# Kernel optimization log

Hardware: AMD Instinct MI355X
Metric: run time of the kernel (lower is better)

The kernel has to match this reference:

```python
import jax, jax.numpy as jnp
import numpy as np

B, S, D = 4, 2048, 1024
NH, NKV = 16, 4
HD = D // NH  # 64


def _rope(x, freqs):
    # x: [B, H, S, HD], freqs: [B, S, HD//2]
    cos = jnp.concatenate([jnp.cos(freqs), jnp.cos(freqs)], axis=-1)[:, None]  # [B,1,S,HD]
    sin = jnp.concatenate([jnp.sin(freqs), jnp.sin(freqs)], axis=-1)[:, None]
    x1, x2 = x[..., : HD // 2], x[..., HD // 2:]
    rot = jnp.concatenate([-x2, x1], axis=-1)
    return x * cos + rot * sin


def setup_inputs() -> dict:
    key = jax.random.key(0)
    ks = jax.random.split(key, 9)
    return {
        "hidden_states": jax.random.normal(ks[0], (B, S, D), jnp.float32),
        "rotary_pos_emb": jax.random.normal(ks[1], (B, S, HD // 2), jnp.float32),
        "Wq": jax.random.normal(ks[2], (D, NH * HD), jnp.float32) * 0.02,
        "bq": jax.random.normal(ks[3], (NH * HD,), jnp.float32) * 0.02,
        "Wk": jax.random.normal(ks[4], (D, NKV * HD), jnp.float32) * 0.02,
        "bk": jax.random.normal(ks[5], (NKV * HD,), jnp.float32) * 0.02,
        "Wv": jax.random.normal(ks[6], (D, NKV * HD), jnp.float32) * 0.02,
        "bv": jax.random.normal(ks[7], (NKV * HD,), jnp.float32) * 0.02,
        "Wo": jax.random.normal(ks[8], (NH * HD, D), jnp.float32) * 0.02,
    }


def reference(hidden_states, rotary_pos_emb, Wq, bq, Wk, bk, Wv, bv, Wo):
    b, s, _ = hidden_states.shape
    # projections -> [B, H, S, HD]
    q = (hidden_states @ Wq + bq).reshape(b, s, NH, HD).transpose(0, 2, 1, 3)
    k = (hidden_states @ Wk + bk).reshape(b, s, NKV, HD).transpose(0, 2, 1, 3)
    v = (hidden_states @ Wv + bv).reshape(b, s, NKV, HD).transpose(0, 2, 1, 3)
    q = _rope(q, rotary_pos_emb)
    k = _rope(k, rotary_pos_emb)
    groups = NH // NKV
    k = jnp.repeat(k, groups, axis=1)  # [B, NH, S, HD]
    v = jnp.repeat(v, groups, axis=1)
    scaling = HD ** -0.5
    scores = jnp.einsum("bhqd,bhkd->bhqk", q, k) * scaling
    probs = jax.nn.softmax(scores.astype(jnp.float32), axis=-1).astype(q.dtype)
    out = jnp.einsum("bhqk,bhkd->bhqd", probs, v)
    out = out.transpose(0, 2, 1, 3).reshape(b, s, NH * HD)
    return out @ Wo
```

## Files before the change

### kernel.cpp

```cpp
#include <hip/hip_runtime.h>
#include <hip/hip_bf16.h>

#define BB 4
#define SS 2048
#define DD 1024
#define NH 16
#define NKV 4
#define HD 64
#define MROWS (BB*SS)
#define NQKV (NH*HD + 2*NKV*HD)
#define KOFF (NH*HD)

typedef short v8s __attribute__((ext_vector_type(8)));
typedef short v4s __attribute__((ext_vector_type(4)));
typedef float v4f __attribute__((ext_vector_type(4)));
typedef unsigned short u16;
typedef unsigned int u32;

__device__ __forceinline__ float bf2f(u16 u){
  union { float f; u32 i; } x; x.i = ((u32)u) << 16; return x.f;
}
__device__ __forceinline__ u16 f2bf(float f){
  union { __hip_bfloat16 h; u16 u; } x; x.h = __float2bfloat16(f); return x.u;
}
__device__ __forceinline__ u32 cvtpk(float lo, float hi){
  u32 r;
  asm("v_cvt_pk_bf16_f32 %0, %1, %2" : "=v"(r) : "v"(lo), "v"(hi));
  return r;
}
__device__ __forceinline__ float fmax3(float a, float b, float c){
  return fmaxf(fmaxf(a, b), c);
}
__device__ __forceinline__ void gl_lds16(const u16* g, u16* l){
  __builtin_amdgcn_global_load_lds(
      (const __attribute__((address_space(1))) u32*)g,
      (__attribute__((address_space(3))) u32*)l, 16, 0, 0);
}


__global__ void build_bqkv(const float* __restrict__ Wq, const float* __restrict__ Wk,
                           const float* __restrict__ Wv, const float* __restrict__ bq,
                           const float* __restrict__ bk, const float* __restrict__ bv,
                           u16* __restrict__ Bt, float* __restrict__ bias){
  int idx = blockIdx.x*256 + threadIdx.x;
  int n = idx >> 10, k = idx & 1023;
  float v;
  if (n < 1024)      v = Wq[k*1024 + n];
  else if (n < 1280) v = Wk[k*256 + (n-1024)];
  else               v = Wv[k*256 + (n-1280)];
  Bt[idx] = f2bf(v);
  if (k == 0) bias[n] = (n < 1024) ? bq[n] : (n < 1280 ? bk[n-1024] : bv[n-1280]);
}

__global__ void build_wo(const float* __restrict__ Wo, u16* __restrict__ Bt){
  int idx = blockIdx.x*256 + threadIdx.x;
  int n = idx >> 10, k = idx & 1023;
  Bt[idx] = f2bf(Wo[k*1024 + n]);
}

__global__ void build_trig(const float* __restrict__ fr, float2* __restrict__ trig){
  int i = blockIdx.x*256 + threadIdx.x;
  float f = fr[i];
  float sn, cs; __sincosf(f, &sn, &cs);
  trig[i] = make_float2(cs, sn);
}

__global__ void rope_k(u16* __restrict__ QKV, const float* __restrict__ fr){
  int idx = blockIdx.x*256 + threadIdx.x;
  int d  = idx & 31;
  int hh = (idx >> 5) & 3;
  long row = idx >> 7;
  int col = KOFF + hh*HD + d;
  u16* p = QKV + row*NQKV;
  float x1 = bf2f(p[col]);
  float x2 = bf2f(p[col+32]);
  float f = fr[row*32 + d];
  float sn, cs; __sincosf(f, &sn, &cs);
  p[col]    = f2bf(x1*cs - x2*sn);
  p[col+32] = f2bf(x2*cs + x1*sn);
}


template<bool BIAS, typename IT, typename OT>
__global__ __launch_bounds__(256) void gemm_bt(
    const IT* __restrict__ A, const u16* __restrict__ Bt,
    const float* __restrict__ bias, OT* __restrict__ C,
    int K, int ldc)
{
  __shared__ u16 As[128*32];
  __shared__ u16 Bs[128*32];
  const int tid = threadIdx.x;
  const int wid = tid >> 6, lane = tid & 63;
  const int g = lane >> 4, c = lane & 15;
  const long brow = (long)blockIdx.y * 128;
  const long bcol = (long)blockIdx.x * 128;
  const int wr = (wid >> 1) * 64, wc = (wid & 1) * 64;
  const int srow = tid >> 2;
  const int scol = (tid & 3) * 8;
  const IT*  ga = &A [(brow + srow)*K + scol];
  const u16* gb = &Bt[(bcol + srow)*K + scol];
  u16* la  = &As[(wid*64)*8];
  u16* lb  = &Bs[(wid*64)*8];
  u16* lwa = &As[srow*32 + scol];
  v4f acc[4][4] = {};
  for (int kt = 0; kt < K; kt += 32) {
    __syncthreads();
    gl_lds16(gb + kt,        lb);
    gl_lds16(gb + 64*K + kt, lb + 256*8);
    if constexpr (sizeof(IT) == 4) {
      float4 a0 = *reinterpret_cast<const float4*>(ga + kt);
      float4 a1 = *reinterpret_cast<const float4*>(ga + kt + 4);
      float4 a2 = *reinterpret_cast<const float4*>(ga + (long)64*K + kt);
      float4 a3 = *reinterpret_cast<const float4*>(ga + (long)64*K + kt + 4);
      union { v8s v; u32 w[4]; } p0, p1;
      p0.w[0] = cvtpk(a0.x, a0.y); p0.w[1] = cvtpk(a0.z, a0.w);
      p0.w[2] = cvtpk(a1.x, a1.y); p0.w[3] = cvtpk(a1.z, a1.w);
      p1.w[0] = cvtpk(a2.x, a2.y); p1.w[1] = cvtpk(a2.z, a2.w);
      p1.w[2] = cvtpk(a3.x, a3.y); p1.w[3] = cvtpk(a3.z, a3.w);
      *reinterpret_cast<v8s*>(lwa)          = p0.v;
      *reinterpret_cast<v8s*>(lwa + 64*32)  = p1.v;
    } else {
      gl_lds16((const u16*)ga + kt,        la);
      gl_lds16((const u16*)ga + 64*K + kt, la + 256*8);
    }
    __syncthreads();
    v8s af[4], bf[4];
    #pragma unroll
    for (int m=0;m<4;m++) af[m] = *reinterpret_cast<const v8s*>(&As[(wr + m*16 + c)*32 + g*8]);
    #pragma unroll
    for (int n=0;n<4;n++) bf[n] = *reinterpret_cast<const v8s*>(&Bs[(wc + n*16 + c)*32 + g*8]);
    __builtin_amdgcn_s_setprio(1);
    #pragma unroll
    for (int m=0;m<4;m++)
      #pragma unroll
      for (int n=0;n<4;n++)
        acc[m][n] = __builtin_amdgcn_mfma_f32_16x16x32_bf16(af[m], bf[n], acc[m][n], 0,0,0);
    __builtin_amdgcn_s_setprio(0);
  }
  #pragma unroll
  for (int m=0;m<4;m++)
    #pragma unroll
    for (int n=0;n<4;n++) {
      int col = (int)bcol + wc + n*16 + c;
      float badd = BIAS ? bias[col] : 0.0f;
      #pragma unroll
      for (int r2=0;r2<4;r2++){
        long row = brow + wr + m*16 + g*4 + r2;
        float v = acc[m][n][r2] + badd;
        if constexpr (sizeof(OT)==2) C[row*ldc + col] = (OT)f2bf(v);
        else                         C[row*ldc + col] = (OT)v;
      }
    }
}


__global__ __launch_bounds__(512) void attn_k(const u16* __restrict__ QKV,
                                              const float2* __restrict__ trig,
                                              u16* __restrict__ Out){
  __shared__ u16 Ks[2][64][64];
  __shared__ u16 Vs[2][64][72];
  const int tid = threadIdx.x;
  const int wid = tid >> 6, lane = tid & 63;
  const int g = lane >> 4, c = lane & 15;
  const int qt = blockIdx.x & 7;
  const int bh = blockIdx.x >> 3;
  const int b = bh >> 4, h = bh & 15;
  const int kvh = h >> 2;
  const u16* Qb = QKV + (long)b*SS*NQKV + h*HD;
  const u16* Kb = QKV + (long)b*SS*NQKV + KOFF + kvh*HD;
  const u16* Vb = Kb + NKV*HD;

  const float SCL = 0.125f * 1.44269504088896f;
  v8s qf[2][2];
  #pragma unroll
  for (int qn=0;qn<2;qn++){
    int lrow = qt*256 + wid*32 + qn*16 + c;
    v8s q0 = *reinterpret_cast<const v8s*>(&Qb[(long)lrow*NQKV + g*8]);
    v8s q1 = *reinterpret_cast<const v8s*>(&Qb[(long)lrow*NQKV + 32 + g*8]);
    const float2* tp = trig + ((long)b*SS + lrow)*32 + g*8;
    union { v8s v; u32 w[4]; } a0, a1;
    #pragma unroll
    for (int wi=0;wi<4;wi++){
      float2 ta = tp[2*wi], tb = tp[2*wi+1];
      float x1a = bf2f((u16)q0[2*wi]),   x2a = bf2f((u16)q1[2*wi]);
      float x1b = bf2f((u16)q0[2*wi+1]), x2b = bf2f((u16)q1[2*wi+1]);
      float r0a = (x1a*ta.x - x2a*ta.y) * SCL;
      float r1a = (x2a*ta.x + x1a*ta.y) * SCL;
      float r0b = (x1b*tb.x - x2b*tb.y) * SCL;
      float r1b = (x2b*tb.x + x1b*tb.y) * SCL;
      a0.w[wi] = cvtpk(r0a, r0b);
      a1.w[wi] = cvtpk(r1a, r1b);
    }
    qf[qn][0] = a0.v; qf[qn][1] = a1.v;
  }

  v8s onesf;
  {
    short ov = (c==0) ? (short)0x3F80 : (short)0;
    #pragma unroll
    for (int j=0;j<8;j++) onesf[j] = ov;
  }

  v4f o[2][5] = {};
  float mr[2] = {0.f, 0.f};

  const int kgrow = wid*8 + (lane >> 3);
  const int kgchk = (lane & 7) ^ (lane >> 3);
  const u16* kp = Kb + (long)kgrow*NQKV + kgchk*8;
  u16* kdst0 = &Ks[0][wid*8][0];
  u16* kdst1 = &Ks[1][wid*8][0];

  const int key0 = 2*(tid >> 4);
  const int dg4  = (tid & 15) * 4;
  const int slot0 = 32*(key0>>5) + 8*((key0>>2)&3) + 4*((key0>>4)&1) + (key0&3);
  int vofs[4];
  #pragma unroll
  for (int j=0;j<4;j++){
    int d = dg4 + j;
    int idx = (((slot0>>3) ^ (d>>3)) << 3) | (slot0 & 7);
    vofs[j] = d*72 + idx;
  }
  u16* VsF = &Vs[0][0][0];

  const u16* vp0 = Vb + (long)key0*NQKV + dg4;
  const u16* vp1 = vp0 + NQKV;

  union { v4s v; u32 w[2]; } vr0, vr1;

  {
    gl_lds16(kp, kdst0);
    vr0.v = *reinterpret_cast<const v4s*>(vp0);
    vr1.v = *reinterpret_cast<const v4s*>(vp1);
    #pragma unroll
    for (int j=0;j<4;j++){
      u32 pkd = __builtin_amdgcn_perm(vr1.w[j>>1], vr0.w[j>>1],
                                      (j&1) ? 0x07060302u : 0x05040100u);
      *reinterpret_cast<u32*>(&VsF[vofs[j]]) = pkd;
    }
  }
  __syncthreads();

  int p = 0;
  for (int t = 0; t < SS/64; ++t){
    if (t+1 < SS/64) {
      long off = (long)(t+1)*64*NQKV;
      gl_lds16(kp + off, p ? kdst0 : kdst1);
      vr0.v = *reinterpret_cast<const v4s*>(vp0 + off);
      vr1.v = *reinterpret_cast<const v4s*>(vp1 + off);
    }

    v4f st[4][2];
    #pragma unroll
    for (int qn=0;qn<2;qn++){
      v4f mi = {-mr[qn], -mr[qn], -mr[qn], -mr[qn]};
      #pragma unroll
      for (int km=0;km<4;km++) st[km][qn] = mi;
    }
    #pragma unroll
    for (int ks=0;ks<2;ks++){
      v8s kf[4];
      #pragma unroll
      for (int km=0;km<4;km++)
        kf[km] = *reinterpret_cast<const v8s*>(
            &Ks[p][km*16 + c][(((ks*4 + g) ^ (c & 7)))*8]);
      __builtin_amdgcn_s_setprio(1);
      #pragma unroll
      for (int km=0;km<4;km++)
        #pragma unroll
        for (int qn=0;qn<2;qn++)
          st[km][qn] = __builtin_amdgcn_mfma_f32_16x16x32_bf16(kf[km], qf[qn][ks], st[km][qn], 0,0,0);
      __builtin_amdgcn_s_setprio(0);
    }

    float al[2];
    bool upd[2];
    #pragma unroll
    for (int qn=0;qn<2;qn++){
      float t0 = fmax3(st[0][qn][0], st[0][qn][1], st[0][qn][2]);
      float t1 = fmax3(st[0][qn][3], st[1][qn][0], st[1][qn][1]);
      float t2 = fmax3(st[1][qn][2], st[1][qn][3], st[2][qn][0]);
      float t3 = fmax3(st[2][qn][1], st[2][qn][2], st[2][qn][3]);
      float t4 = fmax3(st[3][qn][0], st[3][qn][1], st[3][qn][2]);
      float mx = fmaxf(fmax3(t0, t1, t2), fmax3(t3, t4, st[3][qn][3]));
      upd[qn] = !__all(mx <= 8.0f);
      al[qn] = 1.0f;
      if (upd[qn]) {
        mx = fmaxf(mx, __shfl_xor(mx, 16));
        mx = fmaxf(mx, __shfl_xor(mx, 32));
        float d = fmaxf(mx, 0.0f);
        al[qn] = __builtin_amdgcn_exp2f(-d);
        mr[qn] += d;
        #pragma unroll
        for (int km=0;km<4;km++)
          #pragma unroll
          for (int r2=0;r2<4;r2++)
            st[km][qn][r2] -= d;
      }
      #pragma unroll
      for (int km=0;km<4;km++)
        #pragma unroll
        for (int r2=0;r2<4;r2++)
          st[km][qn][r2] = __builtin_amdgcn_exp2f(st[km][qn][r2]);
    }

    v8s pa[2][2];
    #pragma unroll
    for (int qm=0;qm<2;qm++)
      #pragma unroll
      for (int ks=0;ks<2;ks++){
        union { v8s v; u32 w[4]; } u;
        u.w[0] = cvtpk(st[2*ks  ][qm][0], st[2*ks  ][qm][1]);
        u.w[1] = cvtpk(st[2*ks  ][qm][2], st[2*ks  ][qm][3]);
        u.w[2] = cvtpk(st[2*ks+1][qm][0], st[2*ks+1][qm][1]);
        u.w[3] = cvtpk(st[2*ks+1][qm][2], st[2*ks+1][qm][3]);
        pa[qm][ks] = u.v;
      }

    if (upd[0] | upd[1]) {
      #pragma unroll
      for (int qm=0;qm<2;qm++)
        #pragma unroll
        for (int r2=0;r2<4;r2++){
          float a = __shfl(al[qm], g*4 + r2);
          #pragma unroll
          for (int dn=0;dn<5;dn++) o[qm][dn][r2] *= a;
        }
    }

    #pragma unroll
    for (int ks=0;ks<2;ks++){
      __builtin_amdgcn_s_setprio(1);
      #pragma unroll
      for (int dn=0;dn<4;dn++){
        int d0 = dn*16 + c;
        v8s vf = *reinterpret_cast<const v8s*>(&Vs[p][d0][(((ks*4+g) ^ (d0>>3)) << 3)]);
        #pragma unroll
        for (int qm=0;qm<2;qm++)
          o[qm][dn] = __builtin_amdgcn_mfma_f32_16x16x32_bf16(pa[qm][ks], vf, o[qm][dn], 0,0,0);
      }
      #pragma unroll
      for (int qm=0;qm<2;qm++)
        o[qm][4] = __builtin_amdgcn_mfma_f32_16x16x32_bf16(pa[qm][ks], onesf, o[qm][4], 0,0,0);
      __builtin_amdgcn_s_setprio(0);
    }

    if (t+1 < SS/64) {
      const int bofs = (p^1) * (64*72);
      #pragma unroll
      for (int j=0;j<4;j++){
        u32 pkd = __builtin_amdgcn_perm(vr1.w[j>>1], vr0.w[j>>1],
                                        (j&1) ? 0x07060302u : 0x05040100u);
        *reinterpret_cast<u32*>(&VsF[bofs + vofs[j]]) = pkd;
      }
    }
    __syncthreads();
    p ^= 1;
  }

  #pragma unroll
  for (int qm=0;qm<2;qm++)
    #pragma unroll
    for (int r2=0;r2<4;r2++){
      float l = __shfl(o[qm][4][r2], lane & 48);
      float inv = 1.0f / l;
      long row = (long)b*SS + qt*256 + wid*32 + qm*16 + g*4 + r2;
      #pragma unroll
      for (int dn=0;dn<4;dn++)
        Out[row*DD + h*HD + dn*16 + c] = f2bf(o[qm][dn][r2] * inv);
    }
}


extern "C" void kernel_launch(void* const* d_in, const int* in_sizes, int n_in,
                              void* d_out, int out_size, void* d_ws, size_t ws_size,
                              hipStream_t stream)
{
  const float* hs = (const float*)d_in[0];
  const float* fr = (const float*)d_in[1];
  const float* Wq = (const float*)d_in[2];
  const float* bq = (const float*)d_in[3];
  const float* Wk = (const float*)d_in[4];
  const float* bk = (const float*)d_in[5];
  const float* Wv = (const float*)d_in[6];
  const float* bv = (const float*)d_in[7];
  const float* Wo = (const float*)d_in[8];
  float* out = (float*)d_out;
  char* ws = (char*)d_ws;

  u16*   Bqkv = (u16*)(ws + 16777216);
  u16*   WoT  = (u16*)(ws + 16777216 + 3145728);
  float* bias = (float*)(ws + 16777216 + 3145728 + 2097152);
  u16*   QKV  = (u16*)(ws + 22028288);
  u16*   AO   = (u16*)(ws + 22028288 + 25165824);
  float2* trig = (float2*)Bqkv;

  build_bqkv<<<6144, 256, 0, stream>>>(Wq, Wk, Wv, bq, bk, bv, Bqkv, bias);
  build_wo  <<<4096, 256, 0, stream>>>(Wo, WoT);
  gemm_bt<true,  float, u16> <<<dim3(NQKV/128, MROWS/128), 256, 0, stream>>>(hs, Bqkv, bias, QKV, DD, NQKV);
  build_trig<<<1024, 256, 0, stream>>>(fr, trig);
  rope_k    <<<MROWS*NKV*32/256, 256, 0, stream>>>(QKV, fr);
  attn_k    <<<BB*NH*(SS/256), 512, 0, stream>>>(QKV, trig, AO);
  gemm_bt<false, u16, float><<<dim3(DD/128, MROWS/128), 256, 0, stream>>>(AO, WoT, nullptr, out, DD, DD);
}
```

Before: 183.0 us.

## Merge prep kernels and process two KV tiles per barrier in attention

The three weight and trig prep kernels become one launch, and trig gets its own workspace slot instead of aliasing Bqkv. The attention kernel drops the async global-to-LDS K load and the XOR swizzle on K, and moves to four LDS buffers. K and V for two tiles are loaded into registers, and two tiles are computed between barriers. This halves the barrier count and merges launches, at the cost of more LDS and registers and a padded, unswizzled K layout that may see bank conflicts.

```diff
diff --git a/kernel.cpp b/kernel.cpp
--- a/kernel.cpp
+++ b/kernel.cpp
@@ -38,31 +38,32 @@
 }
 
 
-__global__ void build_bqkv(const float* __restrict__ Wq, const float* __restrict__ Wk,
+__global__ void prep_fused(const float* __restrict__ Wq, const float* __restrict__ Wk,
                            const float* __restrict__ Wv, const float* __restrict__ bq,
                            const float* __restrict__ bk, const float* __restrict__ bv,
-                           u16* __restrict__ Bt, float* __restrict__ bias){
-  int idx = blockIdx.x*256 + threadIdx.x;
-  int n = idx >> 10, k = idx & 1023;
-  float v;
-  if (n < 1024)      v = Wq[k*1024 + n];
-  else if (n < 1280) v = Wk[k*256 + (n-1024)];
-  else               v = Wv[k*256 + (n-1280)];
-  Bt[idx] = f2bf(v);
-  if (k == 0) bias[n] = (n < 1024) ? bq[n] : (n < 1280 ? bk[n-1024] : bv[n-1280]);
-}
-
-__global__ void build_wo(const float* __restrict__ Wo, u16* __restrict__ Bt){
-  int idx = blockIdx.x*256 + threadIdx.x;
-  int n = idx >> 10, k = idx & 1023;
-  Bt[idx] = f2bf(Wo[k*1024 + n]);
-}
-
-__global__ void build_trig(const float* __restrict__ fr, float2* __restrict__ trig){
-  int i = blockIdx.x*256 + threadIdx.x;
-  float f = fr[i];
-  float sn, cs; __sincosf(f, &sn, &cs);
-  trig[i] = make_float2(cs, sn);
+                           const float* __restrict__ Wo, const float* __restrict__ fr,
+                           u16* __restrict__ Bqkv, float* __restrict__ bias,
+                           u16* __restrict__ WoT, float2* __restrict__ trig){
+  int bid = blockIdx.x;
+  if (bid < 6144) {
+    int idx = bid*256 + threadIdx.x;
+    int n = idx >> 10, k = idx & 1023;
+    float v;
+    if (n < 1024)      v = Wq[k*1024 + n];
+    else if (n < 1280) v = Wk[k*256 + (n-1024)];
+    else               v = Wv[k*256 + (n-1280)];
+    Bqkv[idx] = f2bf(v);
+    if (k == 0) bias[n] = (n < 1024) ? bq[n] : (n < 1280 ? bk[n-1024] : bv[n-1280]);
+  } else if (bid < 6144 + 4096) {
+    int idx = (bid - 6144)*256 + threadIdx.x;
+    int n = idx >> 10, k = idx & 1023;
+    WoT[idx] = f2bf(Wo[k*1024 + n]);
+  } else {
+    int i = (bid - 10240)*256 + threadIdx.x;
+    float f = fr[i];
+    float sn, cs; __sincosf(f, &sn, &cs);
+    trig[i] = make_float2(cs, sn);
+  }
 }
 
 __global__ void rope_k(u16* __restrict__ QKV, const float* __restrict__ fr){
@@ -157,8 +158,8 @@
 __global__ __launch_bounds__(512) void attn_k(const u16* __restrict__ QKV,
                                               const float2* __restrict__ trig,
                                               u16* __restrict__ Out){
-  __shared__ u16 Ks[2][64][64];
-  __shared__ u16 Vs[2][64][72];
+  __shared__ u16 Ks[4][64][72];
+  __shared__ u16 Vs[4][64][72];
   const int tid = threadIdx.x;
   const int wid = tid >> 6, lane = tid & 63;
   const int g = lane >> 4, c = lane & 15;
@@ -204,12 +205,8 @@
   v4f o[2][5] = {};
   float mr[2] = {0.f, 0.f};
 
-  const int kgrow = wid*8 + (lane >> 3);
-  const int kgchk = (lane & 7) ^ (lane >> 3);
-  const u16* kp = Kb + (long)kgrow*NQKV + kgchk*8;
-  u16* kdst0 = &Ks[0][wid*8][0];
-  u16* kdst1 = &Ks[1][wid*8][0];
-
+  const int krow = tid >> 3;
+  const int kcol = (tid & 7) * 8;
   const int key0 = 2*(tid >> 4);
   const int dg4  = (tid & 15) * 4;
   const int slot0 = 32*(key0>>5) + 8*((key0>>2)&3) + 4*((key0>>4)&1) + (key0&3);
@@ -222,33 +219,26 @@
   }
   u16* VsF = &Vs[0][0][0];
 
+  const u16* kp  = Kb + (long)krow*NQKV + kcol;
   const u16* vp0 = Vb + (long)key0*NQKV + dg4;
   const u16* vp1 = vp0 + NQKV;
 
-  union { v4s v; u32 w[2]; } vr0, vr1;
-
-  {
-    gl_lds16(kp, kdst0);
-    vr0.v = *reinterpret_cast<const v4s*>(vp0);
-    vr1.v = *reinterpret_cast<const v4s*>(vp1);
+  v8s kregA, kregB;
+  union { v4s v; u32 w[2]; } vrA0, vrA1, vrB0, vrB1;
+
+  auto write_tile = [&](int q, const v8s& kr,
+                        const u32* wA, const u32* wB){
+    *reinterpret_cast<v8s*>(&Ks[q][krow][kcol]) = kr;
+    const int bofs = q * (64*72);
     #pragma unroll
     for (int j=0;j<4;j++){
-      u32 pkd = __builtin_amdgcn_perm(vr1.w[j>>1], vr0.w[j>>1],
+      u32 pkd = __builtin_amdgcn_perm(wB[j>>1], wA[j>>1],
                                       (j&1) ? 0x07060302u : 0x05040100u);
-      *reinterpret_cast<u32*>(&VsF[vofs[j]]) = pkd;
-    }
-  }
-  __syncthreads();
-
-  int p = 0;
-  for (int t = 0; t < SS/64; ++t){
-    if (t+1 < SS/64) {
-      long off = (long)(t+1)*64*NQKV;
-      gl_lds16(kp + off, p ? kdst0 : kdst1);
-      vr0.v = *reinterpret_cast<const v4s*>(vp0 + off);
-      vr1.v = *reinterpret_cast<const v4s*>(vp1 + off);
-    }
-
+      *reinterpret_cast<u32*>(&VsF[bofs + vofs[j]]) = pkd;
+    }
+  };
+
+  auto tile_body = [&](int buf){
     v4f st[4][2];
     #pragma unroll
     for (int qn=0;qn<2;qn++){
@@ -261,8 +251,7 @@
       v8s kf[4];
       #pragma unroll
       for (int km=0;km<4;km++)
-        kf[km] = *reinterpret_cast<const v8s*>(
-            &Ks[p][km*16 + c][(((ks*4 + g) ^ (c & 7)))*8]);
+        kf[km] = *reinterpret_cast<const v8s*>(&Ks[buf][km*16 + c][ks*32 + g*8]);
       __builtin_amdgcn_s_setprio(1);
       #pragma unroll
       for (int km=0;km<4;km++)
@@ -333,7 +322,7 @@
       #pragma unroll
       for (int dn=0;dn<4;dn++){
         int d0 = dn*16 + c;
-        v8s vf = *reinterpret_cast<const v8s*>(&Vs[p][d0][(((ks*4+g) ^ (d0>>3)) << 3)]);
+        v8s vf = *reinterpret_cast<const v8s*>(&Vs[buf][d0][(((ks*4+g) ^ (d0>>3)) << 3)]);
         #pragma unroll
         for (int qm=0;qm<2;qm++)
           o[qm][dn] = __builtin_amdgcn_mfma_f32_16x16x32_bf16(pa[qm][ks], vf, o[qm][dn], 0,0,0);
@@ -343,18 +332,43 @@
         o[qm][4] = __builtin_amdgcn_mfma_f32_16x16x32_bf16(pa[qm][ks], onesf, o[qm][4], 0,0,0);
       __builtin_amdgcn_s_setprio(0);
     }
-
-    if (t+1 < SS/64) {
-      const int bofs = (p^1) * (64*72);
-      #pragma unroll
-      for (int j=0;j<4;j++){
-        u32 pkd = __builtin_amdgcn_perm(vr1.w[j>>1], vr0.w[j>>1],
-                                        (j&1) ? 0x07060302u : 0x05040100u);
-        *reinterpret_cast<u32*>(&VsF[bofs + vofs[j]]) = pkd;
-      }
+  };
+
+  {
+    long off1 = (long)64*NQKV;
+    kregA  = *reinterpret_cast<const v8s*>(kp);
+    vrA0.v = *reinterpret_cast<const v4s*>(vp0);
+    vrA1.v = *reinterpret_cast<const v4s*>(vp1);
+    kregB  = *reinterpret_cast<const v8s*>(kp  + off1);
+    vrB0.v = *reinterpret_cast<const v4s*>(vp0 + off1);
+    vrB1.v = *reinterpret_cast<const v4s*>(vp1 + off1);
+    write_tile(0, kregA, vrA0.w, vrA1.w);
+    write_tile(1, kregB, vrB0.w, vrB1.w);
+  }
+  __syncthreads();
+
+  for (int j = 0; j < SS/128; ++j){
+    const int base = (j & 1) * 2;
+    const bool pf = (j + 1 < SS/128);
+    if (pf) {
+      long offA = (long)(2*j+2)*64*NQKV;
+      long offB = (long)(2*j+3)*64*NQKV;
+      kregA  = *reinterpret_cast<const v8s*>(kp  + offA);
+      vrA0.v = *reinterpret_cast<const v4s*>(vp0 + offA);
+      vrA1.v = *reinterpret_cast<const v4s*>(vp1 + offA);
+      kregB  = *reinterpret_cast<const v8s*>(kp  + offB);
+      vrB0.v = *reinterpret_cast<const v4s*>(vp0 + offB);
+      vrB1.v = *reinterpret_cast<const v4s*>(vp1 + offB);
+    }
+
+    tile_body(base);
+    tile_body(base + 1);
+
+    if (pf) {
+      write_tile(base ^ 2,       kregA, vrA0.w, vrA1.w);
+      write_tile((base ^ 2) + 1, kregB, vrB0.w, vrB1.w);
     }
     __syncthreads();
-    p ^= 1;
   }
 
   #pragma unroll
@@ -387,17 +401,16 @@
   float* out = (float*)d_out;
   char* ws = (char*)d_ws;
 
+  float2* trig = (float2*)ws;
   u16*   Bqkv = (u16*)(ws + 16777216);
   u16*   WoT  = (u16*)(ws + 16777216 + 3145728);
   float* bias = (float*)(ws + 16777216 + 3145728 + 2097152);
   u16*   QKV  = (u16*)(ws + 22028288);
   u16*   AO   = (u16*)(ws + 22028288 + 25165824);
-  float2* trig = (float2*)Bqkv;
-
-  build_bqkv<<<6144, 256, 0, stream>>>(Wq, Wk, Wv, bq, bk, bv, Bqkv, bias);
-  build_wo  <<<4096, 256, 0, stream>>>(Wo, WoT);
+
+  prep_fused<<<11264, 256, 0, stream>>>(Wq, Wk, Wv, bq, bk, bv, Wo, fr,
+                                        Bqkv, bias, WoT, trig);
   gemm_bt<true,  float, u16> <<<dim3(NQKV/128, MROWS/128), 256, 0, stream>>>(hs, Bqkv, bias, QKV, DD, NQKV);
-  build_trig<<<1024, 256, 0, stream>>>(fr, trig);
   rope_k    <<<MROWS*NKV*32/256, 256, 0, stream>>>(QKV, fr);
   attn_k    <<<BB*NH*(SS/256), 512, 0, stream>>>(QKV, trig, AO);
   gemm_bt<false, u16, float><<<dim3(DD/128, MROWS/128), 256, 0, stream>>>(AO, WoT, nullptr, out, DD, DD);
```

New measurement: 173.5 us. 5.2% less time.
